# Kernel optimization log

Measured on AMD Instinct MI355X. Metric: run time of the kernel, lower is better.

The kernel has to match this reference:

```python
import jax, jax.numpy as jnp
import numpy as np
import math

INPUT_DIM = 1024
QUERY_DIM = 1024
VALUE_DIM = 1024

def setup_inputs() -> dict:
    key = jax.random.key(0)
    ks = jax.random.split(key, 7)
    N, T, D = 4, 4096, INPUT_DIM
    s_in = 1.0 / math.sqrt(D)
    X = jax.random.normal(ks[0], (N, T, D), dtype=jnp.float32)
    # torch.nn.Linear weights: (out, in), init ~ U(-1/sqrt(in), 1/sqrt(in))
    Wq = jax.random.uniform(ks[1], (QUERY_DIM, D), jnp.float32, -s_in, s_in)
    bq = jax.random.uniform(ks[2], (QUERY_DIM,), jnp.float32, -s_in, s_in)
    Wk = jax.random.uniform(ks[3], (QUERY_DIM, D), jnp.float32, -s_in, s_in)
    bk = jax.random.uniform(ks[4], (QUERY_DIM,), jnp.float32, -s_in, s_in)
    Wv = jax.random.uniform(ks[5], (VALUE_DIM, D), jnp.float32, -s_in, s_in)
    bv = jax.random.uniform(ks[6], (VALUE_DIM,), jnp.float32, -s_in, s_in)
    return {"X": X, "Wq": Wq, "bq": bq, "Wk": Wk, "bk": bk, "Wv": Wv, "bv": bv}

def reference(X, Wq, bq, Wk, bk, Wv, bv):
    N, T, D = X.shape
    q = jnp.einsum('ntd,qd->ntq', X, Wq) + bq  # (N,T,Q)
    k = jnp.einsum('ntd,qd->ntq', X, Wk) + bk  # (N,T,Q)
    v = jnp.einsum('ntd,vd->ntv', X, Wv) + bv  # (N,T,V)
    # NOTE: original scales by sqrt(D) = sqrt(input_dim), not sqrt(query_dim)
    scores = jnp.einsum('ntq,nsq->nts', q, k) / jnp.sqrt(jnp.asarray(D, X.dtype))
    attn = jax.nn.softmax(scores, axis=-1)  # (N,T,T)
    return jnp.einsum('nts,nsv->ntv', attn, v)
```

## Files before the change

kernel.cpp:

```cpp
#include <hip/hip_runtime.h>
#include <stdint.h>

typedef unsigned short u16;
typedef unsigned char u8;
typedef unsigned int u32;
typedef short shortx8 __attribute__((ext_vector_type(8)));
typedef float floatx4 __attribute__((ext_vector_type(4)));
typedef int intx4 __attribute__((ext_vector_type(4)));
typedef int intx8 __attribute__((ext_vector_type(8)));

__device__ __forceinline__ u16 f2bf(float f) {
    u32 u = __builtin_bit_cast(u32, f);
    u = (u + 0x7fffu + ((u >> 16) & 1u)) >> 16;
    return (u16)u;
}

#if defined(__has_builtin)
#  if __has_builtin(__builtin_amdgcn_cvt_pk_fp8_f32)
#    define HAVE_CVT_FP8 1
#  endif
#  if __has_builtin(__builtin_amdgcn_global_load_lds)
#    define HAVE_GLL 1
#  endif
#endif
#ifndef HAVE_CVT_FP8
#  define HAVE_CVT_FP8 0
#endif
#ifndef HAVE_GLL
#  define HAVE_GLL 0
#endif

__device__ __forceinline__ u8 f2fp8(float f) {
#if HAVE_CVT_FP8
    return (u8)(__builtin_amdgcn_cvt_pk_fp8_f32(f, f, 0, false) & 0xff);
#else
    u32 u = __builtin_bit_cast(u32, f);
    u32 s = (u >> 24) & 0x80u;
    u32 m = u & 0x7fffffffu;
    if (m >= 0x43e00000u) return (u8)(s | 0x7eu);
    if (m < 0x3c800000u) {
        int q = __float2int_rn(__builtin_bit_cast(float, m) * 512.f);
        return (u8)(s | (u32)q);
    }
    u32 r = m + 0x7ffffu + ((m >> 20) & 1u);
    u32 code = (((r >> 23) - 120u) << 3) | ((r >> 20) & 7u);
    if (code > 0x7eu) code = 0x7eu;
    return (u8)(s | code);
#endif
}

#if HAVE_GLL
__device__ __forceinline__ void gload_lds16(const void* g, void* l) {
    __builtin_amdgcn_global_load_lds(
        (const __attribute__((address_space(1))) u32*)g,
        (__attribute__((address_space(3))) u32*)l,
        16, 0, 0);
}
#endif

template <typename OutT, int MODE, int SWZ>
__global__ __launch_bounds__(256, 2) void gemm_bt(
    const u16* __restrict__ Ag, const u16* __restrict__ Bg, OutT* __restrict__ Cg,
    int lda, int ldb, int ldc, int K,
    const float* __restrict__ aux, float scale,
    long long sAz, long long sBz, long long sCz, long long sXz,
    int swz_nhalf)
{
    __shared__ u16 smem[4][128 * 32];

    int z, mb, nb;
    if constexpr (SWZ) {
        const int f = blockIdx.x, xcd = f & 7, g = f >> 3;
        z = xcd >> 1;
        mb = g & 31;
        nb = (xcd & 1) * swz_nhalf + (g >> 5);
    } else {
        z = blockIdx.z; mb = blockIdx.y; nb = blockIdx.x;
    }
    const int m0 = mb * 128, n0 = nb * 128;

    const u16* A = Ag + (long long)z * sAz;
    const u16* B = Bg + (long long)z * sBz;
    OutT* C = Cg + (long long)z * sCz;
    const float* auxp = aux ? aux + (long long)z * sXz : nullptr;

    const int tid = threadIdx.x, lane = tid & 63, wv = tid >> 6;

    const int srow = lane >> 2;
    const int schunk = (lane & 3) * 8;
    const u16* gA0 = A + (size_t)(m0 + wv * 16 + srow) * lda + schunk;
    const u16* gA1 = gA0 + (size_t)64 * lda;
    const u16* gB0 = B + (size_t)(n0 + wv * 16 + srow) * ldb + schunk;
    const u16* gB1 = gB0 + (size_t)64 * ldb;
    const int wb = wv * 512;

    const int wm = (wv & 1) * 64, wn = (wv >> 1) * 64;
    const int mi = lane & 15, kq = lane >> 4;

    floatx4 acc[4][4] = {};

    for (int k0 = 0; k0 < K; k0 += 64) {
#if HAVE_GLL
        gload_lds16(gA0,      &smem[0][wb]);
        gload_lds16(gA1,      &smem[0][2048 + wb]);
        gload_lds16(gA0 + 32, &smem[1][wb]);
        gload_lds16(gA1 + 32, &smem[1][2048 + wb]);
        gload_lds16(gB0,      &smem[2][wb]);
        gload_lds16(gB1,      &smem[2][2048 + wb]);
        gload_lds16(gB0 + 32, &smem[3][wb]);
        gload_lds16(gB1 + 32, &smem[3][2048 + wb]);
#else
        *(shortx8*)(&smem[0][wb] + lane * 8)        = *(const shortx8*)gA0;
        *(shortx8*)(&smem[0][2048 + wb] + lane * 8) = *(const shortx8*)gA1;
        *(shortx8*)(&smem[1][wb] + lane * 8)        = *(const shortx8*)(gA0 + 32);
        *(shortx8*)(&smem[1][2048 + wb] + lane * 8) = *(const shortx8*)(gA1 + 32);
        *(shortx8*)(&smem[2][wb] + lane * 8)        = *(const shortx8*)gB0;
        *(shortx8*)(&smem[2][2048 + wb] + lane * 8) = *(const shortx8*)gB1;
        *(shortx8*)(&smem[3][wb] + lane * 8)        = *(const shortx8*)(gB0 + 32);
        *(shortx8*)(&smem[3][2048 + wb] + lane * 8) = *(const shortx8*)(gB1 + 32);
#endif
        gA0 += 64; gA1 += 64; gB0 += 64; gB1 += 64;
        __syncthreads();

#pragma unroll
        for (int h = 0; h < 2; h++) {
            const u16* Ap = smem[h];
            const u16* Bp = smem[2 + h];
            shortx8 af[4], bfr[4];
#pragma unroll
            for (int i = 0; i < 4; i++)
                af[i] = *(const shortx8*)(Ap + (wm + i * 16 + mi) * 32 + kq * 8);
#pragma unroll
            for (int j = 0; j < 4; j++)
                bfr[j] = *(const shortx8*)(Bp + (wn + j * 16 + mi) * 32 + kq * 8);
#pragma unroll
            for (int i = 0; i < 4; i++)
#pragma unroll
                for (int j = 0; j < 4; j++)
                    acc[i][j] = __builtin_amdgcn_mfma_f32_16x16x32_bf16(
                        af[i], bfr[j], acc[i][j], 0, 0, 0);
        }
        __syncthreads();
    }

    float cb[4];
    if constexpr (MODE == 1) {
#pragma unroll
        for (int j = 0; j < 4; j++) cb[j] = auxp[n0 + wn + j * 16 + mi];
    }

    if constexpr (sizeof(OutT) == 2) {
        u16* ct = &smem[0][0];
#pragma unroll
        for (int i = 0; i < 4; i++) {
#pragma unroll
            for (int r = 0; r < 4; r++) {
                const int lrow = wm + i * 16 + kq * 4 + r;
                float radd = 0.f;
                if constexpr (MODE == 2) radd = auxp[m0 + lrow];
#pragma unroll
                for (int j = 0; j < 4; j++) {
                    float v = acc[i][j][r];
                    if constexpr (MODE == 1) v += cb[j];
                    if constexpr (MODE == 2) v += radd;
                    ct[lrow * 128 + wn + j * 16 + mi] = f2bf(v);
                }
            }
        }
        __syncthreads();
#pragma unroll
        for (int it = 0; it < 8; it++) {
            const int fl = (it * 256 + tid) * 8;
            const int row = fl >> 7, col = fl & 127;
            *(uint4*)(C + (size_t)(m0 + row) * ldc + n0 + col) =
                *(const uint4*)(ct + fl);
        }
    } else if constexpr (sizeof(OutT) == 1) {
        u8* ct = (u8*)&smem[0][0];
#pragma unroll
        for (int i = 0; i < 4; i++) {
#pragma unroll
            for (int r = 0; r < 4; r++) {
                const int lrow = wm + i * 16 + kq * 4 + r;
#pragma unroll
                for (int j = 0; j < 4; j++) {
                    float v = acc[i][j][r];
                    if constexpr (MODE == 1) v += cb[j];
                    ct[lrow * 128 + wn + j * 16 + mi] = f2fp8(v);
                }
            }
        }
        __syncthreads();
        u8* base = (u8*)Cg + ((size_t)mb * 16 + nb) * 16384;
#pragma unroll
        for (int it = 0; it < 4; it++) {
            const int fl = (it * 256 + tid) * 16;
            const int row = fl >> 7, c = (fl >> 4) & 7;
            *(uint4*)(base + row * 128 + ((c ^ (row & 7)) << 4)) =
                *(const uint4*)(ct + fl);
        }
    } else {
#pragma unroll
        for (int i = 0; i < 4; i++) {
#pragma unroll
            for (int r = 0; r < 4; r++) {
                const int row = m0 + wm + i * 16 + kq * 4 + r;
                float rmul = 1.f;
                if constexpr (MODE == 4) rmul = 1.0f / auxp[row];
                OutT* crow = C + (size_t)row * ldc;
#pragma unroll
                for (int j = 0; j < 4; j++) {
                    const int col = n0 + wn + j * 16 + mi;
                    crow[col] = acc[i][j][r] * rmul;
                }
            }
        }
    }
}

__global__ __launch_bounds__(512, 2) void gemm_pv256(
    const u16* __restrict__ Pg, const u16* __restrict__ Vt,
    float* __restrict__ outg, const float* __restrict__ sums, int T, int NT)
{
    __shared__ u8 smem[2][65536];

    const int f = blockIdx.x, xcd = f & 7, g = f >> 3;
    const int z = xcd >> 1;
    const int nb = (xcd & 1) * 2 + (g >> 4);
    const int mb = g & 15;
    const int m0 = mb * 256, n0 = nb * 256;

    const u8* Pz = (const u8*)(Pg + (size_t)z * T * T);
    const u8* Vz = (const u8*)(Vt + (size_t)z * T);
    const float* sumz = sums + (size_t)z * T;

    const int tid = threadIdx.x, lane = tid & 63, wv = tid >> 6;
    const int wr = wv >> 2, wc = wv & 3;
    const int mi = lane & 15, kq = lane >> 4;

    const int srow = lane >> 3;
    const int schunk = ((lane & 7) ^ srow) << 4;
    const size_t ldPb = (size_t)T * 2, ldVb = (size_t)NT * 2;
    const u8* gsrc;
    size_t grstride;
    int lds_r0;
    if (wv < 4) {
        gsrc = Pz + (size_t)(m0 + wv * 64 + srow) * ldPb + schunk;
        grstride = ldPb * 8;
        lds_r0 = wv * 8192;
    } else {
        gsrc = Vz + (size_t)(n0 + (wv - 4) * 64 + srow) * ldVb + schunk;
        grstride = ldVb * 8;
        lds_r0 = 32768 + (wv - 4) * 8192;
    }

    const int csw0 = ((0 * 4 + kq) ^ (mi & 7)) << 4;
    const int csw1 = ((1 * 4 + kq) ^ (mi & 7)) << 4;

    floatx4 acc[8][4] = {};

    auto stage = [&](int slot, int kt) {
        const u8* s0 = gsrc + (size_t)kt * 128;
        u8* l0 = &smem[slot][lds_r0];
#if HAVE_GLL
#pragma unroll
        for (int q = 0; q < 8; q++)
            gload_lds16(s0 + (size_t)q * grstride, l0 + q * 1024);
#else
#pragma unroll
        for (int q = 0; q < 8; q++)
            *(uint4*)(l0 + q * 1024 + lane * 16) =
                *(const uint4*)(s0 + (size_t)q * grstride);
#endif
    };

    stage(0, 0);
    __syncthreads();

    for (int kt = 0; kt < 64; kt++) {
        const int s = kt & 1;
        if (kt < 63) stage(s ^ 1, kt + 1);
        __builtin_amdgcn_sched_barrier(0);

        const u8* Ab = &smem[s][0];
        const u8* Bb = &smem[s][32768];

        shortx8 bfr[4][2];
#pragma unroll
        for (int nj = 0; nj < 4; nj++) {
            const u8* p = Bb + (wc * 64 + nj * 16 + mi) * 128;
            bfr[nj][0] = *(const shortx8*)(p + csw0);
            bfr[nj][1] = *(const shortx8*)(p + csw1);
        }
#pragma unroll
        for (int mh = 0; mh < 2; mh++) {
            shortx8 af[4][2];
#pragma unroll
            for (int fi = 0; fi < 4; fi++) {
                const u8* p = Ab + (wr * 128 + (mh * 4 + fi) * 16 + mi) * 128;
                af[fi][0] = *(const shortx8*)(p + csw0);
                af[fi][1] = *(const shortx8*)(p + csw1);
            }
            __builtin_amdgcn_s_setprio(1);
#pragma unroll
            for (int ks = 0; ks < 2; ks++)
#pragma unroll
                for (int fi = 0; fi < 4; fi++)
#pragma unroll
                    for (int nj = 0; nj < 4; nj++)
                        acc[mh * 4 + fi][nj] = __builtin_amdgcn_mfma_f32_16x16x32_bf16(
                            af[fi][ks], bfr[nj][ks], acc[mh * 4 + fi][nj], 0, 0, 0);
            __builtin_amdgcn_s_setprio(0);
        }
        __syncthreads();
    }

#pragma unroll
    for (int fr = 0; fr < 8; fr++) {
#pragma unroll
        for (int r = 0; r < 4; r++) {
            const int row = m0 + wr * 128 + fr * 16 + kq * 4 + r;
            const float rmul = 1.0f / sumz[row];
            float* crow = outg + ((size_t)z * T + row) * 1024 + n0 + wc * 64 + mi;
#pragma unroll
            for (int nj = 0; nj < 4; nj++)
                crow[nj * 16] = acc[fr][nj][r] * rmul;
        }
    }
}

__device__ __forceinline__ intx8 cat8(intx4 a, intx4 b) {
    return __builtin_shufflevector(a, b, 0, 1, 2, 3, 4, 5, 6, 7);
}

template <int SWZ>
__global__ __launch_bounds__(256, 1) void gemm_fp8_scores(
    const u8* __restrict__ QKt, u16* __restrict__ Pg,
    float* __restrict__ sums, float scale, int T)
{
    __shared__ u8 smem[4][32768];

    int z, mb, nb;
    if constexpr (SWZ) {
        const int f = blockIdx.x, xcd = f & 7, g = f >> 3;
        z = xcd >> 1;
        const int s = g >> 7, t = g & 127;
        mb = (s << 3) | (t & 7);
        nb = (xcd & 1) * 16 + (t >> 3);
    } else {
        z = blockIdx.z; mb = blockIdx.y; nb = blockIdx.x;
    }
    const int m0 = mb * 128, n0 = nb * 128;

    const u8* At = QKt + ((size_t)(z * 32 + mb) * 16) * 16384;
    const u8* Bt = QKt + ((size_t)(z * 32 + nb) * 16 + 8) * 16384;
    u16* P = Pg + (size_t)z * T * T;
    float* sumz = sums + (size_t)z * T;

    const int tid = threadIdx.x, lane = tid & 63, wv = tid >> 6;
    const int wm = (wv & 1) * 64, wn = (wv >> 1) * 64;
    const int mi = lane & 15, kq = lane >> 4;
    const int xm = mi & 7;
    const int off0 = ((2 * kq) ^ xm) * 16;
    const int off1 = ((2 * kq + 1) ^ xm) * 16;

    const u8* gA = At + wv * 4096 + lane * 16;
    const u8* gB = Bt + wv * 4096 + lane * 16;

    floatx4 acc[4][4] = {};

    auto stageP = [&](int b) {
#if HAVE_GLL
#pragma unroll
        for (int i = 0; i < 4; i++) {
            gload_lds16(gA + i * 1024, &smem[b][wv * 4096] + i * 1024);
            gload_lds16(gB + i * 1024, &smem[b][16384 + wv * 4096] + i * 1024);
        }
#else
#pragma unroll
        for (int i = 0; i < 4; i++) {
            *(uint4*)(&smem[b][wv * 4096] + i * 1024 + lane * 16) =
                *(const uint4*)(gA + i * 1024);
            *(uint4*)(&smem[b][16384 + wv * 4096] + i * 1024 + lane * 16) =
                *(const uint4*)(gB + i * 1024);
        }
#endif
        gA += 16384; gB += 16384;
    };

    stageP(0);
    stageP(1);
    stageP(2);

#pragma unroll
    for (int kp = 0; kp < 8; kp++) {
#if HAVE_GLL
        if (kp <= 5)      asm volatile("s_waitcnt vmcnt(16)" ::: "memory");
        else if (kp == 6) asm volatile("s_waitcnt vmcnt(8)" ::: "memory");
        else              asm volatile("s_waitcnt vmcnt(0)" ::: "memory");
        __builtin_amdgcn_s_barrier();
#else
        __syncthreads();
#endif
        if (kp < 5) stageP((kp + 3) & 3);
        __builtin_amdgcn_sched_barrier(0);

        const u8* Ap = &smem[kp & 3][0];
        const u8* Bp = &smem[kp & 3][16384];
        intx8 af[4];
#pragma unroll
        for (int i = 0; i < 4; i++) {
            const u8* p = Ap + (wm + i * 16 + mi) * 128;
            af[i] = cat8(*(const intx4*)(p + off0), *(const intx4*)(p + off1));
        }
#pragma unroll
        for (int j = 0; j < 4; j++) {
            const u8* p = Bp + (wn + j * 16 + mi) * 128;
            const intx8 bfr = cat8(*(const intx4*)(p + off0), *(const intx4*)(p + off1));
#pragma unroll
            for (int i = 0; i < 4; i++)
                acc[i][j] = __builtin_amdgcn_mfma_scale_f32_16x16x128_f8f6f4(
                    af[i], bfr, acc[i][j], 0, 0,
                    0, 0x7f7f7f7f, 0, 0x7f7f7f7f);
        }
    }

    u16* ct = (u16*)&smem[0][0];
#pragma unroll
    for (int i = 0; i < 4; i++) {
#pragma unroll
        for (int r = 0; r < 4; r++) {
            const int lrow = wm + i * 16 + kq * 4 + r;
            float rs = 0.f;
#pragma unroll
            for (int j = 0; j < 4; j++) {
                float v = __expf(acc[i][j][r] * scale);
                rs += v;
                ct[lrow * 128 + wn + j * 16 + mi] = f2bf(v);
            }
            rs += __shfl_xor(rs, 1);
            rs += __shfl_xor(rs, 2);
            rs += __shfl_xor(rs, 4);
            rs += __shfl_xor(rs, 8);
            if (mi == 0) atomicAdd(&sumz[m0 + lrow], rs);
        }
    }
    __syncthreads();
#pragma unroll
    for (int it = 0; it < 8; it++) {
        const int fl = (it * 256 + tid) * 8;
        const int row = fl >> 7, col = fl & 127;
        *(uint4*)(P + (size_t)(m0 + row) * T + n0 + col) = *(const uint4*)(ct + fl);
    }
}

__global__ __launch_bounds__(256) void cvt_bf16(const float* __restrict__ s,
                                                u16* __restrict__ d, int n8)
{
    int i = blockIdx.x * 256 + threadIdx.x;
    if (i >= n8) return;
    const float4* sp = (const float4*)s;
    float4 a = sp[2 * i], b = sp[2 * i + 1];
    uint4 o;
    o.x = (u32)f2bf(a.x) | ((u32)f2bf(a.y) << 16);
    o.y = (u32)f2bf(a.z) | ((u32)f2bf(a.w) << 16);
    o.z = (u32)f2bf(b.x) | ((u32)f2bf(b.y) << 16);
    o.w = (u32)f2bf(b.z) | ((u32)f2bf(b.w) << 16);
    *(uint4*)(d + 8 * i) = o;
}

__global__ void concat2(const float* __restrict__ a, const float* __restrict__ b,
                        float* __restrict__ d, int n)
{
    int i = blockIdx.x * 256 + threadIdx.x;
    if (i < n) d[i] = a[i];
    else if (i < 2 * n) d[i] = b[i - n];
}

extern "C" void kernel_launch(void* const* d_in, const int* in_sizes, int n_in,
                              void* d_out, int out_size, void* d_ws, size_t ws_size,
                              hipStream_t stream)
{
    const float* X  = (const float*)d_in[0];
    const float* Wq = (const float*)d_in[1];
    const float* bq = (const float*)d_in[2];
    const float* Wk = (const float*)d_in[3];
    const float* bk = (const float*)d_in[4];
    const float* Wv = (const float*)d_in[5];
    const float* bv = (const float*)d_in[6];
    float* out = (float*)d_out;

    const int T = 4096, NT = 4 * T;
    const long long TL = T;

    char* ws = (char*)d_ws;
    size_t off = 0;
    auto alloc = [&](size_t bytes) {
        char* p = ws + off;
        off += (bytes + 255) & ~(size_t)255;
        return p;
    };
    u16*   Wqk  = (u16*)alloc((size_t)2048 * 1024 * 2);
    u16*   Wvb  = (u16*)alloc((size_t)1024 * 1024 * 2);
    float* bqk  = (float*)alloc(2048 * 4);
    u8*    QKt  = (u8*)alloc((size_t)128 * 16 * 16384);
    u16*   Vt   = (u16*)alloc((size_t)1024 * NT * 2);
    float* sums = (float*)alloc((size_t)NT * 4);
    size_t pbase = off;
    u16*   Xb   = (u16*)alloc((size_t)NT * 1024 * 2);
    u16*   P    = Xb;

    const size_t need_batched = pbase + (size_t)4 * T * T * 2;
    const bool batched = ws_size >= need_batched;

    cvt_bf16<<<dim3((NT * 1024 / 8 + 255) / 256), dim3(256), 0, stream>>>(X, Xb, NT * 1024 / 8);
    cvt_bf16<<<dim3(512), dim3(256), 0, stream>>>(Wq, Wqk, 1024 * 1024 / 8);
    cvt_bf16<<<dim3(512), dim3(256), 0, stream>>>(Wk, Wqk + 1024 * 1024, 1024 * 1024 / 8);
    cvt_bf16<<<dim3(512), dim3(256), 0, stream>>>(Wv, Wvb, 1024 * 1024 / 8);
    concat2<<<dim3(8), dim3(256), 0, stream>>>(bq, bk, bqk, 1024);
    hipMemsetAsync(sums, 0, (size_t)NT * 4, stream);

    gemm_bt<u8, 1, 0><<<dim3(16, 128, 1), dim3(256), 0, stream>>>(
        Xb, Wqk, QKt, 1024, 1024, 0, 1024, bqk, 0.f, 0, 0, 0, 0, 0);

    gemm_bt<u16, 2, 0><<<dim3(128, 8, 1), dim3(256), 0, stream>>>(
        Wvb, Xb, Vt, 1024, 1024, NT, 1024, bv, 0.f, 0, 0, 0, 0, 0);

    if (batched) {
        gemm_fp8_scores<1><<<dim3(4096), dim3(256), 0, stream>>>(
            QKt, P, sums, 0.03125f, T);
        gemm_pv256<<<dim3(256), dim3(512), 0, stream>>>(
            P, Vt, out, sums, T, NT);
    } else {
        for (int z = 0; z < 4; z++) {
            gemm_fp8_scores<0><<<dim3(32, 32, 1), dim3(256), 0, stream>>>(
                QKt + (size_t)z * 32 * 16 * 16384, P, sums + (size_t)z * T, 0.03125f, T);
            gemm_bt<float, 4, 0><<<dim3(8, 32, 1), dim3(256), 0, stream>>>(
                P, Vt + (size_t)z * T, out + (size_t)z * T * 1024,
                T, NT, 1024, T, sums + (size_t)z * T, 0.f, 0, 0, 0, 0, 0);
        }
    }
    (void)in_sizes; (void)n_in; (void)out_size;
}
```

Measured before the change: 495.1 us.

## Restructure FP8 scores kernel to 8 waves with double-buffered LDS

Changes the FP8 QK^T scores kernel from 4 waves with a 4-deep LDS pipeline to 8 waves (512 threads) with a 2-deep double buffer. Each wave now owns a 32x64 output subtile, which halves the accumulator registers per wave. LDS drops to 64KB, so launch bounds now ask for higher occupancy. The fine-grained vmcnt waits are replaced with a __syncthreads per k-step. This trades explicit deep prefetch for latency hiding through more waves, at the cost of extra barriers and a shallower pipeline.

```diff
diff --git a/kernel.cpp b/kernel.cpp
--- a/kernel.cpp
+++ b/kernel.cpp
@@ -334,11 +334,11 @@
 }
 
 template <int SWZ>
-__global__ __launch_bounds__(256, 1) void gemm_fp8_scores(
+__global__ __launch_bounds__(512, 4) void gemm_fp8_scores(
     const u8* __restrict__ QKt, u16* __restrict__ Pg,
     float* __restrict__ sums, float scale, int T)
 {
-    __shared__ u8 smem[4][32768];
+    __shared__ u8 smem[2][32768];
 
     int z, mb, nb;
     if constexpr (SWZ) {
@@ -358,58 +358,45 @@
     float* sumz = sums + (size_t)z * T;
 
     const int tid = threadIdx.x, lane = tid & 63, wv = tid >> 6;
-    const int wm = (wv & 1) * 64, wn = (wv >> 1) * 64;
+    const int wm = (wv >> 1) * 32, wn = (wv & 1) * 64;
     const int mi = lane & 15, kq = lane >> 4;
     const int xm = mi & 7;
     const int off0 = ((2 * kq) ^ xm) * 16;
     const int off1 = ((2 * kq + 1) ^ xm) * 16;
 
-    const u8* gA = At + wv * 4096 + lane * 16;
-    const u8* gB = Bt + wv * 4096 + lane * 16;
-
-    floatx4 acc[4][4] = {};
+    const u8* gA = At + wv * 2048 + lane * 16;
+    const u8* gB = Bt + wv * 2048 + lane * 16;
+
+    floatx4 acc[2][4] = {};
 
     auto stageP = [&](int b) {
 #if HAVE_GLL
-#pragma unroll
-        for (int i = 0; i < 4; i++) {
-            gload_lds16(gA + i * 1024, &smem[b][wv * 4096] + i * 1024);
-            gload_lds16(gB + i * 1024, &smem[b][16384 + wv * 4096] + i * 1024);
-        }
+        gload_lds16(gA,        &smem[b][wv * 2048]);
+        gload_lds16(gA + 1024, &smem[b][wv * 2048 + 1024]);
+        gload_lds16(gB,        &smem[b][16384 + wv * 2048]);
+        gload_lds16(gB + 1024, &smem[b][16384 + wv * 2048 + 1024]);
 #else
-#pragma unroll
-        for (int i = 0; i < 4; i++) {
-            *(uint4*)(&smem[b][wv * 4096] + i * 1024 + lane * 16) =
-                *(const uint4*)(gA + i * 1024);
-            *(uint4*)(&smem[b][16384 + wv * 4096] + i * 1024 + lane * 16) =
-                *(const uint4*)(gB + i * 1024);
-        }
+        *(uint4*)(&smem[b][wv * 2048] + lane * 16)         = *(const uint4*)gA;
+        *(uint4*)(&smem[b][wv * 2048 + 1024] + lane * 16)  = *(const uint4*)(gA + 1024);
+        *(uint4*)(&smem[b][16384 + wv * 2048] + lane * 16) = *(const uint4*)gB;
+        *(uint4*)(&smem[b][16384 + wv * 2048 + 1024] + lane * 16) = *(const uint4*)(gB + 1024);
 #endif
         gA += 16384; gB += 16384;
     };
 
     stageP(0);
-    stageP(1);
-    stageP(2);
-
-#pragma unroll
+    __syncthreads();
+
     for (int kp = 0; kp < 8; kp++) {
-#if HAVE_GLL
-        if (kp <= 5)      asm volatile("s_waitcnt vmcnt(16)" ::: "memory");
-        else if (kp == 6) asm volatile("s_waitcnt vmcnt(8)" ::: "memory");
-        else              asm volatile("s_waitcnt vmcnt(0)" ::: "memory");
-        __builtin_amdgcn_s_barrier();
-#else
-        __syncthreads();
-#endif
-        if (kp < 5) stageP((kp + 3) & 3);
+        const int cur = kp & 1;
+        if (kp < 7) stageP(cur ^ 1);
         __builtin_amdgcn_sched_barrier(0);
 
-        const u8* Ap = &smem[kp & 3][0];
-        const u8* Bp = &smem[kp & 3][16384];
-        intx8 af[4];
-#pragma unroll
-        for (int i = 0; i < 4; i++) {
+        const u8* Ap = &smem[cur][0];
+        const u8* Bp = &smem[cur][16384];
+        intx8 af[2];
+#pragma unroll
+        for (int i = 0; i < 2; i++) {
             const u8* p = Ap + (wm + i * 16 + mi) * 128;
             af[i] = cat8(*(const intx4*)(p + off0), *(const intx4*)(p + off1));
         }
@@ -418,16 +405,17 @@
             const u8* p = Bp + (wn + j * 16 + mi) * 128;
             const intx8 bfr = cat8(*(const intx4*)(p + off0), *(const intx4*)(p + off1));
 #pragma unroll
-            for (int i = 0; i < 4; i++)
+            for (int i = 0; i < 2; i++)
                 acc[i][j] = __builtin_amdgcn_mfma_scale_f32_16x16x128_f8f6f4(
                     af[i], bfr, acc[i][j], 0, 0,
                     0, 0x7f7f7f7f, 0, 0x7f7f7f7f);
         }
+        __syncthreads();
     }
 
     u16* ct = (u16*)&smem[0][0];
 #pragma unroll
-    for (int i = 0; i < 4; i++) {
+    for (int i = 0; i < 2; i++) {
 #pragma unroll
         for (int r = 0; r < 4; r++) {
             const int lrow = wm + i * 16 + kq * 4 + r;
@@ -447,8 +435,8 @@
     }
     __syncthreads();
 #pragma unroll
-    for (int it = 0; it < 8; it++) {
-        const int fl = (it * 256 + tid) * 8;
+    for (int it = 0; it < 4; it++) {
+        const int fl = (it * 512 + tid) * 8;
         const int row = fl >> 7, col = fl & 127;
         *(uint4*)(P + (size_t)(m0 + row) * T + n0 + col) = *(const uint4*)(ct + fl);
     }
@@ -527,13 +515,13 @@
         Wvb, Xb, Vt, 1024, 1024, NT, 1024, bv, 0.f, 0, 0, 0, 0, 0);
 
     if (batched) {
-        gemm_fp8_scores<1><<<dim3(4096), dim3(256), 0, stream>>>(
+        gemm_fp8_scores<1><<<dim3(4096), dim3(512), 0, stream>>>(
             QKt, P, sums, 0.03125f, T);
         gemm_pv256<<<dim3(256), dim3(512), 0, stream>>>(
             P, Vt, out, sums, T, NT);
     } else {
         for (int z = 0; z < 4; z++) {
-            gemm_fp8_scores<0><<<dim3(32, 32, 1), dim3(256), 0, stream>>>(
+            gemm_fp8_scores<0><<<dim3(32, 32, 1), dim3(512), 0, stream>>>(
                 QKt + (size_t)z * 32 * 16 * 16384, P, sums + (size_t)z * T, 0.03125f, T);
             gemm_bt<float, 4, 0><<<dim3(8, 32, 1), dim3(256), 0, stream>>>(
                 P, Vt + (size_t)z * T, out + (size_t)z * T * 1024,
```

Result: slower. 539.3 us (+8.9%).
